# Optimization experiments

Measured on AMD Instinct MI355X. Metric: run time of the kernel, lower is better.

## Reference

```python
import jax, jax.numpy as jnp
from jax import lax
import numpy as np

B, T, L = 8, 24, 145
DHID, DFRAME, DEMB, DGCN, V = 1024, 2500, 128, 512, 1024
PF = 300
DINP = DHID + DFRAME + DEMB + DGCN   # 4164 = LSTM input size
DCONT = DHID + DINP                  # 5188 = cont_t size
FLAT = 64 * 7 * 7                    # 3136
BN_EPS = 1e-5
BN_INV = float(1.0 / np.sqrt(1.0 + BN_EPS))  # eval BN with running mean 0, var 1


def setup_inputs() -> dict:
    key = jax.random.key(0)
    ks = iter(jax.random.split(key, 48))
    rn = lambda *s: jax.random.normal(next(ks), s, jnp.float32)
    w = lambda *s: 0.02 * rn(*s)
    return dict(
        enc=rn(B, L, DHID),
        frames=rn(B, T, 512, 7, 7),
        gcn_embedding=rn(B, DGCN),
        h0=jnp.zeros((B, DHID), jnp.float32),
        c0=jnp.zeros((B, DHID), jnp.float32),
        conv1_w=w(256, 512), conv1_b=jnp.zeros((256,), jnp.float32),
        bn1_g=jnp.ones((256,), jnp.float32), bn1_b=jnp.zeros((256,), jnp.float32),
        conv2_w=w(64, 256), conv2_b=jnp.zeros((64,), jnp.float32),
        bn2_g=jnp.ones((64,), jnp.float32), bn2_b=jnp.zeros((64,), jnp.float32),
        fc_w=w(DFRAME, FLAT), fc_b=jnp.zeros((DFRAME,), jnp.float32),
        hfc_w=w(DHID, DHID), hfc_b=jnp.zeros((DHID,), jnp.float32),
        w_ih=w(4 * DHID, DINP), w_hh=w(4 * DHID, DHID),
        b_ih=jnp.zeros((4 * DHID,), jnp.float32), b_hh=jnp.zeros((4 * DHID,), jnp.float32),
        go=0.1 * rn(DEMB),
        emb_w=w(V, DEMB),
        actor_w=w(DEMB, DCONT), actor_b=jnp.zeros((DEMB,), jnp.float32),
        d1_w=w(FLAT, DCONT), d1_b=jnp.zeros((FLAT,), jnp.float32),
        dconv3_w=w(64, 32, 4, 4), dconv3_b=jnp.zeros((32,), jnp.float32),
        bnm2_g=jnp.ones((32,), jnp.float32), bnm2_b=jnp.zeros((32,), jnp.float32),
        dconv2_w=w(32, 16, 4, 4), dconv2_b=jnp.zeros((16,), jnp.float32),
        bnm1_g=jnp.ones((16,), jnp.float32), bnm1_b=jnp.zeros((16,), jnp.float32),
        dconv1_w=w(16, 1, 4, 4), dconv1_b=jnp.zeros((1,), jnp.float32),
    )


def _bn_eval(x, g, b):
    # BatchNorm2d in eval mode with running_mean=0, running_var=1
    return g[None, :, None, None] * (x * BN_INV) + b[None, :, None, None]


def _up2(x):
    # UpsamplingNearest2d(scale_factor=2)
    return jnp.repeat(jnp.repeat(x, 2, axis=2), 2, axis=3)


def _deconv(x, w, b):
    # ConvTranspose2d(k=4, s=2, p=1); torch weight layout (in, out, kH, kW)
    k = jnp.flip(w, (2, 3)).transpose(1, 0, 2, 3)  # -> (out, in, kH, kW)
    y = lax.conv_general_dilated(x, k, window_strides=(1, 1), padding=((2, 2), (2, 2)),
                                 lhs_dilation=(2, 2),
                                 dimension_numbers=('NCHW', 'OIHW', 'NCHW'))
    return y + b[None, :, None, None]


def reference(enc, frames, gcn_embedding, h0, c0,
              conv1_w, conv1_b, bn1_g, bn1_b, conv2_w, conv2_b, bn2_g, bn2_b, fc_w, fc_b,
              hfc_w, hfc_b, w_ih, w_hh, b_ih, b_hh, go, emb_w, actor_w, actor_b,
              d1_w, d1_b, dconv3_w, dconv3_b, bnm2_g, bnm2_b,
              dconv2_w, dconv2_b, bnm1_g, bnm1_b, dconv1_w, dconv1_b):

    def vis_encode(frame):  # [B,512,7,7] -> [B,DFRAME]
        x = jnp.einsum('bchw,oc->bohw', frame, conv1_w) + conv1_b[None, :, None, None]
        x = jax.nn.relu(_bn_eval(x, bn1_g, bn1_b))
        x = jnp.einsum('bchw,oc->bohw', x, conv2_w) + conv2_b[None, :, None, None]
        x = jax.nn.relu(_bn_eval(x, bn2_g, bn2_b))
        return x.reshape(-1, FLAT) @ fc_w.T + fc_b

    def mask_decode(cont):  # [B,DCONT] -> [B,1,300,300]
        x = jax.nn.relu(cont @ d1_w.T + d1_b).reshape(-1, 64, 7, 7)
        x = _deconv(_up2(x), dconv3_w, dconv3_b)          # 14 -> 28
        x = jax.nn.relu(_bn_eval(x, bnm2_g, bnm2_b))
        x = _deconv(_up2(x), dconv2_w, dconv2_b)          # 56 -> 112
        x = jax.nn.relu(_bn_eval(x, bnm1_g, bnm1_b))
        x = _deconv(x, dconv1_w, dconv1_b)                # 112 -> 224
        return jax.image.resize(x, (x.shape[0], 1, PF, PF), method='bilinear')

    def step(carry, frame_t):
        h, c, e_t = carry
        vis = vis_encode(frame_t)
        hq = h @ hfc_w.T + hfc_b
        score = jax.nn.softmax(jnp.einsum('bld,bd->bl', enc, hq), axis=1)  # [B,L]
        weighted = jnp.einsum('bl,bld->bd', score, enc)
        inp = jnp.concatenate([vis, weighted, e_t, gcn_embedding], axis=1)  # [B,DINP]
        gates = inp @ w_ih.T + b_ih + h @ w_hh.T + b_hh
        i, f, g, o = jnp.split(gates, 4, axis=1)
        c_new = jax.nn.sigmoid(f) * c + jax.nn.sigmoid(i) * jnp.tanh(g)
        h_new = jax.nn.sigmoid(o) * jnp.tanh(c_new)
        cont = jnp.concatenate([h_new, inp], axis=1)  # [B,DCONT]
        action = (cont @ actor_w.T + actor_b) @ emb_w.T  # [B,V]
        mask = mask_decode(cont)
        e_new = emb_w[jnp.argmax(action, axis=1)]  # greedy feed-back
        return (h_new, c_new, e_new), (action, mask, score[:, :, None])

    e0 = jnp.tile(go[None, :], (enc.shape[0], 1))
    (h_T, c_T, _), (actions, masks, attns) = lax.scan(
        step, (h0, c0, e0), jnp.swapaxes(frames, 0, 1))
    out_action = jnp.swapaxes(actions, 0, 1)   # [B,T,V]
    out_mask = jnp.swapaxes(masks, 0, 1)       # [B,T,1,300,300]
    out_attn = jnp.swapaxes(attns, 0, 1)       # [B,T,L,1]
    return (out_action, out_mask, out_attn, h_T, c_T)
```

## Files before the change

kernel.cpp:

```cpp
#include <hip/hip_runtime.h>
#include <cstdint>
#include <cstddef>

#define DEV __device__ __forceinline__
typedef short bf16x8 __attribute__((ext_vector_type(8)));
typedef float fl4 __attribute__((ext_vector_type(4)));
typedef float f32x4 __attribute__((ext_vector_type(4)));
typedef unsigned short u16;

#define BN_INV 0.9999950000375f

DEV float b2f(u16 u){ return __uint_as_float(((unsigned)u)<<16); }
DEV u16 f2b(float f){ unsigned u = __float_as_uint(f); unsigned r = (u + 0x7FFFu + ((u>>16)&1u))>>16; return (u16)r; }

DEV bf16x8 load8(const u16* p){ return *(const bf16x8*)p; }
DEV bf16x8 load8(const float* p){
  fl4 a = *(const fl4*)p; fl4 b = *(const fl4*)(p+4);
  bf16x8 r;
  r[0]=(short)f2b(a[0]); r[1]=(short)f2b(a[1]); r[2]=(short)f2b(a[2]); r[3]=(short)f2b(a[3]);
  r[4]=(short)f2b(b[0]); r[5]=(short)f2b(b[1]); r[6]=(short)f2b(b[2]); r[7]=(short)f2b(b[3]);
  return r;
}


__global__ __launch_bounds__(256) void k_pack_frames(const float* __restrict__ fr, u16* __restrict__ XT){
  int bt = blockIdx.x, tid = threadIdx.x;
  for (int e=0;e<128;e++){
    int flat = e*256 + tid;
    int p = flat>>9, c = flat&511;
    u16 v = 0;
    if (p < 49) v = f2b(fr[((size_t)bt*512 + c)*49 + p]);
    XT[((size_t)bt*64 + p)*512 + c] = v;
  }
}

__global__ __launch_bounds__(256) void k_pack_wseq(const float* __restrict__ w_ih, const float* __restrict__ w_hh,
                                                   u16* __restrict__ wseq){
  int r = blockIdx.x, tid = threadIdx.x;
  const float* wr = w_ih + (size_t)r*4164;
  for (int j=tid;j<2176;j+=256){
    float v = (j < 1024) ? w_hh[(size_t)r*1024 + j] : wr[2500 + (j-1024)];
    wseq[(size_t)r*2176 + j] = f2b(v);
  }
}

__global__ __launch_bounds__(256) void k_pack_dseq(const float* __restrict__ d1_w, const float* __restrict__ actor_w,
                                                   u16* __restrict__ dseq){
  int r = blockIdx.x, tid = threadIdx.x;
  const float* wr = (r < 3136) ? (d1_w + (size_t)r*5188) : (actor_w + (size_t)(r-3136)*5188);
  for (int j=tid;j<2176;j+=256){
    float v = (j < 1024) ? wr[j] : wr[3524 + (j-1024)];
    dseq[(size_t)r*2176 + j] = f2b(v);
  }
}

__global__ __launch_bounds__(256) void k_pack_fcw(const float* __restrict__ fc_w, u16* __restrict__ fcwB){
  int r = blockIdx.x, tid = threadIdx.x;
  const float* wr = fc_w + (size_t)r*3136;
  u16* dst = fcwB + (size_t)r*3136;
  for (int j=tid;j<3136;j+=256) dst[j] = f2b(wr[j]);
}

__global__ __launch_bounds__(256) void k_pack_wvg(const float* __restrict__ w_ih, u16* __restrict__ wvg, int rbase){
  int r = rbase + blockIdx.x, tid = threadIdx.x;
  const float* wr = w_ih + (size_t)r*4164;
  u16* dst = wvg + (size_t)blockIdx.x*3072;
  for (int j=tid;j<3072;j+=256){
    float v = 0.f;
    if (j < 2500) v = wr[j];
    else if (j < 3012) v = wr[3652 + (j-2500)];
    dst[j] = f2b(v);
  }
}

__global__ __launch_bounds__(256) void k_pack_dvg(const float* __restrict__ d1_w, const float* __restrict__ actor_w,
                                                  u16* __restrict__ dvg, int rbase){
  int r = rbase + blockIdx.x, tid = threadIdx.x;
  const float* wr = (r < 3136) ? (d1_w + (size_t)r*5188) : (actor_w + (size_t)(r-3136)*5188);
  u16* dst = dvg + (size_t)blockIdx.x*3072;
  for (int j=tid;j<3072;j+=256){
    float v = 0.f;
    if (j < 2500) v = wr[1024 + j];
    else if (j < 3012) v = wr[4676 + (j-2500)];
    dst[j] = f2b(v);
  }
}

__global__ __launch_bounds__(256) void k_hfcT(const float* __restrict__ hfc_w, u16* __restrict__ hfcT){
  int idx = blockIdx.x*256 + threadIdx.x;
  int k = idx>>10, o = idx&1023;
  hfcT[idx] = f2b(hfc_w[o*1024 + k]);
}

DEV u16 wt_map(const float* w, int n, int k, int CIN, int COUT){
  int o = n % COUT; int cls = n / COUT;
  if (cls >= 4) return 0;
  int py = cls>>1, px = cls&1;
  int i = k/9; int dd = k - i*9; int dy = dd/3, dx = dd - dy*3;
  if (i >= CIN) return 0;
  int ky = (py==0) ? (dy==0 ? 3 : (dy==1 ? 1 : -1)) : (dy==1 ? 2 : (dy==2 ? 0 : -1));
  int kx = (px==0) ? (dx==0 ? 3 : (dx==1 ? 1 : -1)) : (dx==1 ? 2 : (dx==2 ? 0 : -1));
  if (ky < 0 || kx < 0) return 0;
  return f2b(w[((i*COUT + o)*4 + ky)*4 + kx]);
}

__global__ __launch_bounds__(256) void k_misc(
  const float* b_ih, const float* b_hh, const float* d1_b, const float* actor_b,
  const float* emb_w, const float* h0, const float* c0,
  const float* dw3, const float* dw2, const float* dw1,
  float* bias_g, float* bias_da, u16* embT, float* hb0, float* cws,
  u16* Wt3, u16* Wt2, u16* Wt1)
{
  int blk = blockIdx.x, tid = threadIdx.x;
  if (blk < 16){ int i = blk*256+tid; if (i<4096) bias_g[i] = b_ih[i] + b_hh[i]; }
  else if (blk < 29){ int i = (blk-16)*256+tid; if (i<3264) bias_da[i] = (i<3136)? d1_b[i] : actor_b[i-3136]; }
  else if (blk < 541){ int i = (blk-29)*256+tid; int j = i>>10, v = i&1023; embT[i] = f2b(emb_w[v*128 + j]); }
  else if (blk < 573){ int i = (blk-541)*256+tid; if (i<8192){ hb0[i] = h0[i]; cws[i] = c0[i]; } }
  else if (blk < 574){ for (int i=tid;i<2560;i+=256){ int n=i/160, k=i-n*160; Wt1[i] = wt_map(dw1,n,k,16,1); } }
  else if (blk < 590){ for (int i=(blk-574)*256+tid; i<18432; i+=16*256){ int n=i/288, k=i-n*288; Wt2[i] = wt_map(dw2,n,k,32,16); } }
  else { for (int i=(blk-590)*256+tid; i<73728; i+=168*256){ int n=i/576, k=i-n*576; Wt3[i] = wt_map(dw3,n,k,64,32); } }
}

__global__ __launch_bounds__(256) void k_eb(const float* __restrict__ enc, const float* __restrict__ hfc_b, float* __restrict__ eb){
  int li = blockIdx.x*4 + (threadIdx.x>>6);
  int lane = threadIdx.x & 63;
  if (li >= 1160) return;
  const float* ep = enc + (size_t)li*1024;
  float a = 0.f;
  for (int k=lane;k<1024;k+=64) a += ep[k]*hfc_b[k];
  #pragma unroll
  for (int off=32; off; off>>=1) a += __shfl_xor(a, off);
  if (lane == 0) eb[li] = a;
}

__global__ __launch_bounds__(256) void k_vis_in(const u16* __restrict__ Y2, u16* __restrict__ vis_in){
  int bt = blockIdx.x, tid = threadIdx.x;
  for (int f=tid; f<3136; f+=256){
    int c = f/49, p = f - c*49;
    vis_in[(size_t)bt*3136 + f] = Y2[((size_t)bt*64 + p)*64 + c];
  }
}

__global__ __launch_bounds__(256) void k_xin(const u16* __restrict__ vis, const float* __restrict__ gcn, u16* __restrict__ xin2){
  int bt = blockIdx.x, tid = threadIdx.x, b = bt/24;
  for (int j=tid;j<3072;j+=256){
    u16 v = 0;
    if (j < 2500) v = vis[(size_t)bt*2500 + j];
    else if (j < 3012) v = f2b(gcn[b*512 + (j-2500)]);
    xin2[(size_t)bt*3072 + j] = v;
  }
}

template<int OUTB, int ACT, typename TA, typename TB>
__global__ __launch_bounds__(256) void gemm64(
  const TA* __restrict__ A, int lda, const TB* __restrict__ Bm, int ldb,
  void* __restrict__ Cv, int ldc, int M, int N, int K,
  const float* __restrict__ bias, const float* __restrict__ cb, const float* __restrict__ gg, const float* __restrict__ bb)
{
  __shared__ u16 sA[64*72];
  __shared__ u16 sB[64*72];
  int tid = threadIdx.x, lane = tid & 63, w = tid >> 6;
  int wm = w & 1, wn = w >> 1;
  int m0 = blockIdx.x*64, n0 = blockIdx.y*64;
  f32x4 acc[2][2];
  #pragma unroll
  for (int a=0;a<2;a++)
    #pragma unroll
    for (int b=0;b<2;b++){ acc[a][b][0]=0;acc[a][b][1]=0;acc[a][b][2]=0;acc[a][b][3]=0; }

  for (int k0=0;k0<K;k0+=64){
    #pragma unroll
    for (int j=0;j<2;j++){
      int c = tid + 256*j; int row = c>>3; int col = (c&7)*8;
      bf16x8 va = {0,0,0,0,0,0,0,0};
      int gm = m0 + row;
      if (gm < M) va = load8(A + (size_t)gm*lda + k0 + col);
      *(bf16x8*)(&sA[row*72 + col]) = va;
      bf16x8 vb = {0,0,0,0,0,0,0,0};
      int gn = n0 + row;
      if (gn < N) vb = load8(Bm + (size_t)gn*ldb + k0 + col);
      *(bf16x8*)(&sB[row*72 + col]) = vb;
    }
    __syncthreads();
    #pragma unroll
    for (int kk=0;kk<2;kk++){
      bf16x8 af[2], bfv[2];
      #pragma unroll
      for (int tm=0;tm<2;tm++) af[tm]  = *(const bf16x8*)(&sA[(wm*32+tm*16+(lane&15))*72 + kk*32 + (lane>>4)*8]);
      #pragma unroll
      for (int tn=0;tn<2;tn++) bfv[tn] = *(const bf16x8*)(&sB[(wn*32+tn*16+(lane&15))*72 + kk*32 + (lane>>4)*8]);
      #pragma unroll
      for (int tm=0;tm<2;tm++)
        #pragma unroll
        for (int tn=0;tn<2;tn++)
          acc[tm][tn] = __builtin_amdgcn_mfma_f32_16x16x32_bf16(af[tm], bfv[tn], acc[tm][tn], 0,0,0);
    }
    __syncthreads();
  }
  int ml = (lane>>4)*4, nl = lane&15;
  #pragma unroll
  for (int tm=0;tm<2;tm++)
    #pragma unroll
    for (int tn=0;tn<2;tn++)
      #pragma unroll
      for (int r=0;r<4;r++){
        int gm = m0 + wm*32 + tm*16 + ml + r;
        int gn = n0 + wn*32 + tn*16 + nl;
        if (gm < M && gn < N){
          float v = acc[tm][tn][r];
          if (ACT == 0){ if (bias) v += bias[gn]; }
          else { v = (v + cb[gn])*BN_INV*gg[gn] + bb[gn]; v = fmaxf(v, 0.f); }
          if (OUTB) ((u16*)Cv)[(size_t)gm*ldc + gn] = f2b(v);
          else      ((float*)Cv)[(size_t)gm*ldc + gn] = v;
        }
      }
}

template<int OUTB, int NMAJOR, typename TA, typename TB>
__global__ __launch_bounds__(64) void gemm16x(
  const TA* __restrict__ A, int lda, const TB* __restrict__ Bm, int ldb,
  void* __restrict__ Cv, int ldc, int M, int N, int K, const float* __restrict__ bias,
  int MT, int NT)
{
  int nb = gridDim.x;
  int orig = blockIdx.x;
  int q = nb >> 3, r = nb & 7;
  int xcd = orig & 7, j = orig >> 3;
  int wg = (xcd < r ? xcd*(q+1) : r*(q+1) + (xcd-r)*q) + j;
  int bx, by;
  if (NMAJOR){ bx = wg % MT; by = wg / MT; }
  else       { by = wg % NT; bx = wg / NT; }
  int lane = threadIdx.x;
  int m0 = bx*16, n0 = by*16;
  int gm = m0 + (lane&15); if (gm > M-1) gm = M-1;
  int gn = n0 + (lane&15); if (gn > N-1) gn = N-1;
  const TA* ap = A  + (size_t)gm*lda + ((lane>>4)*8);
  const TB* bp = Bm + (size_t)gn*ldb + ((lane>>4)*8);
  f32x4 acc = {0,0,0,0};
  #pragma unroll 8
  for (int ks=0; ks<K; ks+=32){
    bf16x8 a = load8(ap + ks);
    bf16x8 b = load8(bp + ks);
    acc = __builtin_amdgcn_mfma_f32_16x16x32_bf16(a, b, acc, 0,0,0);
  }
  int nn = n0 + (lane&15);
  if (nn >= N) return;
  #pragma unroll
  for (int r2=0;r2<4;r2++){
    int mm = m0 + (lane>>4)*4 + r2;
    if (mm < M){
      float v = acc[r2];
      if (bias) v += bias[nn];
      if (OUTB) ((u16*)Cv)[(size_t)mm*ldc + nn] = f2b(v);
      else      ((float*)Cv)[(size_t)mm*ldc + nn] = v;
    }
  }
}


__global__ __launch_bounds__(256) void p1_scores_action(
  const float* __restrict__ encH, const float* __restrict__ eb,
  const float* __restrict__ hcur, const float* __restrict__ cws,
  float* __restrict__ scores, const float* __restrict__ d1a_out,
  const u16* __restrict__ embT, float* __restrict__ out_act,
  float* __restrict__ cmv, int* __restrict__ cmi,
  float* __restrict__ out_h, float* __restrict__ out_c,
  u16* __restrict__ xb1, int t)
{
  __shared__ float shf[1024];
  __shared__ int shi[256];
  int blk = blockIdx.x, tid = threadIdx.x;
  if (blk < 40){
    if (t == 24) return;
    int b = blk & 7, lc = blk >> 3;
    #pragma unroll
    for (int e=0;e<4;e++) shf[tid + 256*e] = hcur[b*1024 + tid + 256*e];
    __syncthreads();
    int w = tid>>6, lane = tid&63;
    for (int i=w;i<29;i+=4){
      int l = lc*29 + i;
      const float* ep = encH + (size_t)(b*145+l)*1024;
      float a = 0.f;
      for (int k=lane;k<1024;k+=64) a += ep[k]*shf[k];
      #pragma unroll
      for (int off=32; off; off>>=1) a += __shfl_xor(a, off);
      if (lane == 0) scores[b*145+l] = a + eb[b*145+l];
    }
  } else if (blk < 72){
    if (t == 0) return;
    int idx = blk-40; int b = idx>>2, vc = idx&3;
    if (tid < 128) shf[tid] = d1a_out[(size_t)(b*24 + t-1)*3264 + 3136 + tid];
    __syncthreads();
    int v = vc*256 + tid;
    float a = 0.f;
    for (int j=0;j<128;j++) a += shf[j]*b2f(embT[j*1024 + v]);
    out_act[(size_t)(b*24 + t-1)*1024 + v] = a;
    shf[256+tid] = a; shi[tid] = v;
    __syncthreads();
    for (int s=128; s; s>>=1){
      if (tid < s){
        float o = shf[256+tid+s]; int oi = shi[tid+s];
        float c = shf[256+tid];   int ci = shi[tid];
        if (o > c || (o == c && oi < ci)){ shf[256+tid] = o; shi[tid] = oi; }
      }
      __syncthreads();
    }
    if (tid == 0){ cmv[b*4+vc] = shf[256]; cmi[b*4+vc] = shi[0]; }
  } else {
    int b = blk-72;
    if (t == 24){
      #pragma unroll
      for (int e=0;e<4;e++){
        int k = tid + 256*e;
        out_h[b*1024+k] = hcur[b*1024+k];
        out_c[b*1024+k] = cws[b*1024+k];
      }
    } else {
      #pragma unroll
      for (int e=0;e<4;e++){
        int k = tid + 256*e;
        xb1[b*2176 + k] = f2b(hcur[b*1024+k]);
      }
    }
  }
}

__global__ __launch_bounds__(256) void p2_softmax_weighted(
  const float* __restrict__ scores, const float* __restrict__ enc,
  float* __restrict__ wgt, float* __restrict__ ecur,
  const float* __restrict__ cmv, const int* __restrict__ cmi,
  const float* __restrict__ emb_w, const float* __restrict__ go,
  float* __restrict__ out_attn, u16* __restrict__ xb1, u16* __restrict__ xb2, int t)
{
  int b = blockIdx.x & 7, dc = blockIdx.x >> 3, tid = threadIdx.x;
  __shared__ float s[145];
  __shared__ float mxs, invs;
  if (tid < 145) s[tid] = scores[b*145+tid];
  __syncthreads();
  if (tid < 64){
    float m = -1e30f;
    for (int i=tid;i<145;i+=64) m = fmaxf(m, s[i]);
    #pragma unroll
    for (int off=32; off; off>>=1) m = fmaxf(m, __shfl_xor(m, off));
    if (tid == 0) mxs = m;
  }
  __syncthreads();
  if (tid < 145) s[tid] = expf(s[tid]-mxs);
  __syncthreads();
  if (tid < 64){
    float sm = 0.f;
    for (int i=tid;i<145;i+=64) sm += s[i];
    #pragma unroll
    for (int off=32; off; off>>=1) sm += __shfl_xor(sm, off);
    if (tid == 0) invs = 1.f/sm;
  }
  __syncthreads();
  float inv = invs;
  if (tid < 128){
    int d = dc*128 + tid;
    float a = 0.f;
    for (int l=0;l<145;l++) a += s[l]*enc[(size_t)(b*145+l)*1024 + d];
    float wv = a*inv;
    wgt[b*1024+d] = wv;
    u16 wb = f2b(wv);
    xb1[b*2176 + 1024 + d] = wb;
    xb2[b*2176 + 1024 + d] = wb;
  } else {
    int i = tid-128;
    if (dc == 0){
      if (i < 145) out_attn[(size_t)(b*24+t)*145 + i] = s[i]*inv;
      int l2 = i + 128;
      if (l2 < 145) out_attn[(size_t)(b*24+t)*145 + l2] = s[l2]*inv;
    } else if (dc == 1){
      float ev;
      if (t == 0) ev = go[i];
      else {
        float bv = cmv[b*4]; int bi = cmi[b*4];
        #pragma unroll
        for (int c=1;c<4;c++){
          float v2 = cmv[b*4+c]; int i2 = cmi[b*4+c];
          if (v2 > bv || (v2 == bv && i2 < bi)){ bv = v2; bi = i2; }
        }
        ev = emb_w[bi*128 + i];
      }
      ecur[b*128+i] = ev;
      u16 eb16 = f2b(ev);
      xb1[b*2176 + 2048 + i] = eb16;
      xb2[b*2176 + 2048 + i] = eb16;
    }
  }
}

__global__ __launch_bounds__(64) void p3m(
  const u16* __restrict__ wseq, const u16* __restrict__ xb, float* __restrict__ gates4)
{
  int orig = blockIdx.x;
  int blk = (orig & 7)*32 + (orig >> 3);
  int lane = threadIdx.x;
  int n = blk*16 + (lane & 15);
  const u16* bp = wseq + (size_t)n*2176 + ((lane>>4)*8);
  const u16* ap = xb + (lane&7)*2176 + ((lane>>4)*8);
  f32x4 acc = {0,0,0,0};
  #pragma unroll 8
  for (int kk=0;kk<68;kk++){
    bf16x8 a = *(const bf16x8*)(ap + kk*32);
    bf16x8 b = *(const bf16x8*)(bp + kk*32);
    acc = __builtin_amdgcn_mfma_f32_16x16x32_bf16(a, b, acc, 0,0,0);
  }
  #pragma unroll
  for (int r=0;r<4;r++){
    int m = (lane>>4)*4 + r;
    if (m < 8) gates4[(size_t)m*4096 + n] = acc[r];
  }
}

__global__ __launch_bounds__(256) void p3l(
  const float* __restrict__ gates4, const float* __restrict__ gpre,
  float* __restrict__ hnew, float* __restrict__ cws, u16* __restrict__ xb2, int t)
{
  int idx = blockIdx.x*256 + threadIdx.x;
  int b = idx>>10, J = idx&1023;
  const float* gp = gpre + (size_t)(b*24+t)*4096;
  const float* gb = gates4 + (size_t)b*4096;
  float iv = gb[J]      + gp[J];
  float fv = gb[1024+J] + gp[1024+J];
  float gv = gb[2048+J] + gp[2048+J];
  float ov = gb[3072+J] + gp[3072+J];
  float ig = 1.f/(1.f+expf(-iv));
  float fg = 1.f/(1.f+expf(-fv));
  float gt = tanhf(gv);
  float og = 1.f/(1.f+expf(-ov));
  float cn = fg*cws[idx] + ig*gt;
  cws[idx] = cn;
  float hv = og*tanhf(cn);
  hnew[idx] = hv;
  xb2[b*2176 + J] = f2b(hv);
}

__global__ __launch_bounds__(64) void p4m(
  const u16* __restrict__ dseq, const u16* __restrict__ xb2,
  const float* __restrict__ dpre, float* __restrict__ dout, int t)
{
  int orig = blockIdx.x;
  int xcd = orig & 7, j = orig >> 3;
  int blk = (xcd < 4 ? xcd*26 : 104 + (xcd-4)*25) + j;
  int lane = threadIdx.x;
  int R = blk*16 + (lane & 15);
  const u16* bp = dseq + (size_t)R*2176 + ((lane>>4)*8);
  const u16* ap = xb2 + (lane&7)*2176 + ((lane>>4)*8);
  f32x4 acc = {0,0,0,0};
  #pragma unroll 8
  for (int kk=0;kk<68;kk++){
    bf16x8 a = *(const bf16x8*)(ap + kk*32);
    bf16x8 b = *(const bf16x8*)(bp + kk*32);
    acc = __builtin_amdgcn_mfma_f32_16x16x32_bf16(a, b, acc, 0,0,0);
  }
  #pragma unroll
  for (int r=0;r<4;r++){
    int m = (lane>>4)*4 + r;
    if (m < 8){
      size_t row = (size_t)(m*24+t)*3264;
      dout[row + R] = acc[r] + dpre[row + R];
    }
  }
}


DEV void stage_tile3(u16* sAt, const float* __restrict__ d1a_bt, int p0, int tid){
  int m = tid & 15;
  int p = p0 + m;
  int u = p / 14, v = p - u*14;
  bool pv = p < 196;
  for (int k = tid>>4; k < 576; k += 16){
    float val = 0.f;
    if (pv){
      int i = k/9; int dd = k - i*9; int dy = dd/3, dx = dd - dy*3;
      int uy = u + dy - 1, vx = v + dx - 1;
      if (uy >= 0 && uy < 14 && vx >= 0 && vx < 14)
        val = fmaxf(d1a_bt[i*49 + (uy>>1)*7 + (vx>>1)], 0.f);
    }
    sAt[m*584 + k] = f2b(val);
  }
}

DEV void stage_tile2(u16* sAt, const float* __restrict__ m1c_bt, int p0, int tid){
  int m = tid & 15;
  int p = p0 + m;
  int u = p / 56, v = p - u*56;
  bool pv = p < 3136;
  for (int k = tid>>4; k < 288; k += 16){
    float val = 0.f;
    if (pv){
      int i = k/9; int dd = k - i*9; int dy = dd/3, dx = dd - dy*3;
      int uy = u + dy - 1, vx = v + dx - 1;
      if (uy >= 0 && uy < 56 && vx >= 0 && vx < 56)
        val = m1c_bt[i*784 + (uy>>1)*28 + (vx>>1)];
    }
    sAt[m*296 + k] = f2b(val);
  }
}

__global__ __launch_bounds__(256) void md3_deconv(const float* __restrict__ d1a_out, int btbase, float* __restrict__ m1c,
  const u16* __restrict__ Wt3, const float* __restrict__ b3, const float* __restrict__ g3, const float* __restrict__ bb3)
{
  __shared__ u16 sAt[16*584];
  int tid = threadIdx.x, lane = tid&63, w = tid>>6;
  int cb = blockIdx.x;
  const float* in_bt = d1a_out + (size_t)(btbase+cb)*3264;
  float* out_bt = m1c + (size_t)cb*32*784;
  int nt = blockIdx.y*4 + w;
  bf16x8 wc[18];
  #pragma unroll
  for (int ks=0;ks<18;ks++) wc[ks] = *(const bf16x8*)(Wt3 + (size_t)(nt*16 + (lane&15))*576 + ks*32 + (lane>>4)*8);
  int cls = nt>>1; int o = (nt&1)*16 + (lane&15);
  int py = cls>>1, px = cls&1;
  float cbv = b3[o], gv = g3[o], bbv = bb3[o];
  int mt = blockIdx.z;
  stage_tile3(sAt, in_bt, mt*16, tid);
  __syncthreads();
  f32x4 acc = {0,0,0,0};
  #pragma unroll
  for (int ks=0;ks<18;ks++){
    bf16x8 a = *(const bf16x8*)(&sAt[(lane&15)*584 + ks*32 + (lane>>4)*8]);
    acc = __builtin_amdgcn_mfma_f32_16x16x32_bf16(a, wc[ks], acc, 0,0,0);
  }
  #pragma unroll
  for (int r=0;r<4;r++){
    int p = mt*16 + (lane>>4)*4 + r;
    if (p < 196){
      int u = p/14, v = p - (p/14)*14;
      float vv = fmaxf((acc[r] + cbv)*BN_INV*gv + bbv, 0.f);
      out_bt[((size_t)o*28 + (2*u+py))*28 + (2*v+px)] = vv;
    }
  }
}

__global__ __launch_bounds__(256) void md2_deconv(const float* __restrict__ m1c, float* __restrict__ m2,
  const u16* __restrict__ Wt2, const float* __restrict__ b2, const float* __restrict__ g2, const float* __restrict__ bb2)
{
  __shared__ u16 sAt[16*296];
  int tid = threadIdx.x, lane = tid&63, w = tid>>6;
  int cb = blockIdx.x;
  const float* in_bt = m1c + (size_t)cb*32*784;
  float* out_bt = m2 + (size_t)cb*16*12544;
  int nt = w;
  bf16x8 wc[9];
  #pragma unroll
  for (int ks=0;ks<9;ks++) wc[ks] = *(const bf16x8*)(Wt2 + (size_t)(nt*16 + (lane&15))*288 + ks*32 + (lane>>4)*8);
  int cls = nt; int o = lane&15;
  int py = cls>>1, px = cls&1;
  float cbv = b2[o], gv = g2[o], bbv = bb2[o];
  int mt = blockIdx.y;
  stage_tile2(sAt, in_bt, mt*16, tid);
  __syncthreads();
  f32x4 acc = {0,0,0,0};
  #pragma unroll
  for (int ks=0;ks<9;ks++){
    bf16x8 a = *(const bf16x8*)(&sAt[(lane&15)*296 + ks*32 + (lane>>4)*8]);
    acc = __builtin_amdgcn_mfma_f32_16x16x32_bf16(a, wc[ks], acc, 0,0,0);
  }
  #pragma unroll
  for (int r=0;r<4;r++){
    int p = mt*16 + (lane>>4)*4 + r;
    if (p < 3136){
      int u = p/56, v = p - u*56;
      float vv = fmaxf((acc[r] + cbv)*BN_INV*gv + bbv, 0.f);
      out_bt[((size_t)o*112 + (2*u+py))*112 + (2*v+px)] = vv;
    }
  }
}

__global__ __launch_bounds__(256) void md1_direct(const float* __restrict__ m2, float* __restrict__ m3,
  const float* __restrict__ dw1, const float* __restrict__ b1)
{
  __shared__ float wl[256];
  int tid = threadIdx.x;
  wl[tid] = dw1[tid];
  __syncthreads();
  int cb = blockIdx.x;
  const float* in_bt = m2 + (size_t)cb*16*12544;
  float* out_bt = m3 + (size_t)cb*50176;
  int idx = blockIdx.y*256 + tid;
  int oy = idx/56, q = idx - oy*56;
  int ox0 = q*4;
  int iyA = (oy+1)>>1;  bool vA = iyA < 112;
  int iyB = iyA - 1;    bool vB = iyB >= 0;
  int kyA = (oy&1) ? 0 : 1;
  int kyB = kyA + 2;
  int xb = (ox0>>1) - 1;
  bool v0 = xb >= 0, v3 = (xb+3) < 112;
  int x0 = v0 ? xb : 0, x3 = v3 ? xb+3 : 111;
  float mA = vA ? 1.f : 0.f, mB = vB ? 1.f : 0.f;
  float mA0 = v0 ? mA : 0.f, mA3 = v3 ? mA : 0.f;
  float mB0 = v0 ? mB : 0.f, mB3 = v3 ? mB : 0.f;
  const float* rA = in_bt + (size_t)(vA ? iyA : 0)*112;
  const float* rB = in_bt + (size_t)(vB ? iyB : 0)*112;
  float acc0=0.f, acc1=0.f, acc2=0.f, acc3=0.f;
  #pragma unroll 4
  for (int i=0;i<16;i++){
    const float* cA = rA + i*12544;
    const float* cB = rB + i*12544;
    float a0 = cA[x0]*mA0, a1 = cA[xb+1]*mA, a2 = cA[xb+2]*mA, a3 = cA[x3]*mA3;
    float b0 = cB[x0]*mB0, b1v = cB[xb+1]*mB, b2 = cB[xb+2]*mB, b3 = cB[x3]*mB3;
    fl4 wA = *(const fl4*)(&wl[i*16 + kyA*4]);
    fl4 wB = *(const fl4*)(&wl[i*16 + kyB*4]);
    acc0 += a1*wA[1] + a0*wA[3] + b1v*wB[1] + b0*wB[3];
    acc1 += a2*wA[0] + a1*wA[2] + b2*wB[0] + b1v*wB[2];
    acc2 += a2*wA[1] + a1*wA[3] + b2*wB[1] + b1v*wB[3];
    acc3 += a3*wA[0] + a2*wA[2] + b3*wB[0] + b2*wB[2];
  }
  float bv = b1[0];
  fl4 o4 = {acc0+bv, acc1+bv, acc2+bv, acc3+bv};
  *(fl4*)(out_bt + (size_t)oy*224 + ox0) = o4;
}

__global__ __launch_bounds__(256) void k_resize(const float* __restrict__ m3, float* __restrict__ out_mask, int btbase){
  int cb = blockIdx.x;
  const float* in_bt = m3 + (size_t)cb*50176;
  int idx = blockIdx.y*256 + threadIdx.x;
  if (idx >= 90000) return;
  int oy = idx/300, ox = idx - oy*300;
  const float sc = 224.f/300.f;
  float sy = (oy+0.5f)*sc - 0.5f;
  float sx = (ox+0.5f)*sc - 0.5f;
  float fy = floorf(sy), fx = floorf(sx);
  float wy = sy-fy, wx = sx-fx;
  int y0 = (int)fy, x0 = (int)fx;
  int y0c = min(max(y0,0),223), y1c = min(max(y0+1,0),223);
  int x0c = min(max(x0,0),223), x1c = min(max(x0+1,0),223);
  float v00 = in_bt[y0c*224+x0c], v01 = in_bt[y0c*224+x1c];
  float v10 = in_bt[y1c*224+x0c], v11 = in_bt[y1c*224+x1c];
  float v = (1.f-wy)*((1.f-wx)*v00 + wx*v01) + wy*((1.f-wx)*v10 + wx*v11);
  out_mask[(size_t)(btbase+cb)*90000 + idx] = v;
}


extern "C" void kernel_launch(void* const* d_in, const int* in_sizes, int n_in,
                              void* d_out, int out_size, void* d_ws, size_t ws_size,
                              hipStream_t stream)
{
  const float* enc      = (const float*)d_in[0];
  const float* frames   = (const float*)d_in[1];
  const float* gcn      = (const float*)d_in[2];
  const float* h0       = (const float*)d_in[3];
  const float* c0       = (const float*)d_in[4];
  const float* conv1_w  = (const float*)d_in[5];
  const float* conv1_b  = (const float*)d_in[6];
  const float* bn1_g    = (const float*)d_in[7];
  const float* bn1_b    = (const float*)d_in[8];
  const float* conv2_w  = (const float*)d_in[9];
  const float* conv2_b  = (const float*)d_in[10];
  const float* bn2_g    = (const float*)d_in[11];
  const float* bn2_b    = (const float*)d_in[12];
  const float* fc_w     = (const float*)d_in[13];
  const float* fc_b     = (const float*)d_in[14];
  const float* hfc_w    = (const float*)d_in[15];
  const float* hfc_b    = (const float*)d_in[16];
  const float* w_ih     = (const float*)d_in[17];
  const float* w_hh     = (const float*)d_in[18];
  const float* b_ih     = (const float*)d_in[19];
  const float* b_hh     = (const float*)d_in[20];
  const float* go       = (const float*)d_in[21];
  const float* emb_w    = (const float*)d_in[22];
  const float* actor_w  = (const float*)d_in[23];
  const float* actor_b  = (const float*)d_in[24];
  const float* d1_w     = (const float*)d_in[25];
  const float* d1_b     = (const float*)d_in[26];
  const float* dconv3_w = (const float*)d_in[27];
  const float* dconv3_b = (const float*)d_in[28];
  const float* bnm2_g   = (const float*)d_in[29];
  const float* bnm2_b   = (const float*)d_in[30];
  const float* dconv2_w = (const float*)d_in[31];
  const float* dconv2_b = (const float*)d_in[32];
  const float* bnm1_g   = (const float*)d_in[33];
  const float* bnm1_b   = (const float*)d_in[34];
  const float* dconv1_w = (const float*)d_in[35];
  const float* dconv1_b = (const float*)d_in[36];
  (void)in_sizes; (void)n_in; (void)out_size;

  float* obase    = (float*)d_out;
  float* out_act  = obase;
  float* out_mask = obase + 196608;
  float* out_attn = obase + 17476608;
  float* out_h    = obase + 17504448;
  float* out_c    = obase + 17512640;

  char* ob = (char*)out_mask;
  size_t ooff = 0;
  auto oalloc = [&](size_t bytes)->char*{ char* p = ob + ooff; ooff = (ooff + bytes + 255) & ~(size_t)255; return p; };
  u16*   wseq      = (u16*)  oalloc(4096ULL*2176*2);
  u16*   dseq      = (u16*)  oalloc(3264ULL*2176*2);
  float* encH      = (float*)oalloc(1160ULL*1024*4);
  float* gates_pre = (float*)oalloc(192ULL*4096*4);
  float* d1a_pre   = (float*)oalloc(192ULL*3264*4);
  u16*   xin2      = (u16*)  oalloc(192ULL*3072*2);
  u16*   XT     = (u16*)oalloc(12288ULL*512*2);
  u16*   Y1     = (u16*)oalloc(12288ULL*256*2);
  u16*   Y2     = (u16*)oalloc(12288ULL*64*2);
  u16*   vis_in = (u16*)oalloc(192ULL*3136*2);
  u16*   vis    = (u16*)oalloc(192ULL*2500*2);
  u16*   wchunk = XT;
  u16*   fcwB   = XT;

  char* wsb = (char*)d_ws;
  size_t off = 0;
  auto alloc = [&](size_t bytes)->char*{ char* p = wsb + off; off = (off + bytes + 255) & ~(size_t)255; return p; };
  float* d1a_out   = (float*)alloc(192ULL*3264*4);
  u16*   embT      = (u16*)  alloc(128ULL*1024*2);
  float* eb        = (float*)alloc(1160ULL*4);
  u16*   Wt3       = (u16*)  alloc(128ULL*576*2);
  u16*   Wt2       = (u16*)  alloc(64ULL*288*2);
  u16*   Wt1       = (u16*)  alloc(16ULL*160*2);
  float* hb        = (float*)alloc(2ULL*8192*4);
  float* c_ws      = (float*)alloc(8192ULL*4);
  float* e_cur     = (float*)alloc(8ULL*128*4);
  float* weighted  = (float*)alloc(8192ULL*4);
  float* scores_raw= (float*)alloc(8ULL*145*4);
  float* cmv       = (float*)alloc(32ULL*4);
  int*   cmi       = (int*)  alloc(32ULL*4);
  float* bias_g    = (float*)alloc(4096ULL*4);
  float* bias_da   = (float*)alloc(3264ULL*4);
  u16*   xb1       = (u16*)  alloc(8ULL*2176*2);
  u16*   xb2       = (u16*)  alloc(8ULL*2176*2);
  float* gates4    = (float*)alloc(8ULL*4096*4);
  size_t zbase = off;
  u16*   hfcT = (u16*)alloc(1024ULL*1024*2);

  const int cands[10] = {48,24,16,12,8,6,4,3,2,1};
  int C = 1;
  for (int i=0;i<10;i++){
    size_t need = zbase + (size_t)cands[i]*1103872ULL + 65536;
    if (need <= ws_size){ C = cands[i]; break; }
  }
  size_t mo = zbase;
  auto malloc_ = [&](size_t bytes)->char*{ char* p = wsb + mo; mo = (mo + bytes + 255) & ~(size_t)255; return p; };
  float* m1c  = (float*)malloc_((size_t)C*32*784*4);
  float* m2b  = (float*)malloc_((size_t)C*16*12544*4);
  float* m3b  = (float*)malloc_((size_t)C*50176*4);

  k_pack_frames<<<192, 256, 0, stream>>>(frames, XT);
  k_pack_wseq<<<4096, 256, 0, stream>>>(w_ih, w_hh, wseq);
  k_pack_dseq<<<3264, 256, 0, stream>>>(d1_w, actor_w, dseq);
  k_hfcT<<<4096, 256, 0, stream>>>(hfc_w, hfcT);
  k_misc<<<758, 256, 0, stream>>>(b_ih, b_hh, d1_b, actor_b, emb_w, h0, c0,
                                  dconv3_w, dconv2_w, dconv1_w,
                                  bias_g, bias_da, embT, hb, c_ws, Wt3, Wt2, Wt1);
  k_eb<<<290, 256, 0, stream>>>(enc, hfc_b, eb);

  gemm64<1,1><<<dim3(192,4), 256, 0, stream>>>(XT, 512, conv1_w, 512, Y1, 256, 12288, 256, 512, nullptr, conv1_b, bn1_g, bn1_b);
  gemm64<1,1><<<dim3(192,1), 256, 0, stream>>>(Y1, 256, conv2_w, 256, Y2, 64, 12288, 64, 256, nullptr, conv2_b, bn2_g, bn2_b);
  k_vis_in<<<192, 256, 0, stream>>>(Y2, vis_in);
  k_pack_fcw<<<2500, 256, 0, stream>>>(fc_w, fcwB);
  gemm16x<1,1><<<12*157, 64, 0, stream>>>(vis_in, 3136, fcwB, 3136, vis, 2500, 192, 2500, 3136, fc_b, 12, 157);
  k_xin<<<192, 256, 0, stream>>>(vis, gcn, xin2);
  gemm16x<0,0><<<73*64, 64, 0, stream>>>(enc, 1024, hfcT, 1024, encH, 1024, 1160, 1024, 1024, nullptr, 73, 64);

  for (int c=0;c<2;c++){
    k_pack_wvg<<<2048, 256, 0, stream>>>(w_ih, wchunk, c*2048);
    gemm16x<0,1><<<12*128, 64, 0, stream>>>(xin2, 3072, wchunk, 3072, gates_pre + c*2048, 4096,
                                            192, 2048, 3072, bias_g + c*2048, 12, 128);
  }
  for (int c=0;c<2;c++){
    k_pack_dvg<<<1632, 256, 0, stream>>>(d1_w, actor_w, wchunk, c*1632);
    gemm16x<0,1><<<12*102, 64, 0, stream>>>(xin2, 3072, wchunk, 3072, d1a_pre + c*1632, 3264,
                                            192, 1632, 3072, bias_da + c*1632, 12, 102);
  }

  for (int t=0; t<=24; t++){
    float* hcur = hb + (t&1)*8192;
    float* hnew = hb + ((t+1)&1)*8192;
    p1_scores_action<<<80, 256, 0, stream>>>(encH, eb, hcur, c_ws, scores_raw, d1a_out, embT,
                                             out_act, cmv, cmi, out_h, out_c, xb1, t);
    if (t == 24) break;
    p2_softmax_weighted<<<64, 256, 0, stream>>>(scores_raw, enc, weighted, e_cur, cmv, cmi, emb_w, go,
                                                out_attn, xb1, xb2, t);
    p3m<<<256, 64, 0, stream>>>(wseq, xb1, gates4);
    p3l<<<32, 256, 0, stream>>>(gates4, gates_pre, hnew, c_ws, xb2, t);
    p4m<<<204, 64, 0, stream>>>(dseq, xb2, d1a_pre, d1a_out, t);
  }

  for (int btbase=0; btbase<192; btbase+=C){
    md3_deconv<<<dim3(C,2,13), 256, 0, stream>>>(d1a_out, btbase, m1c, Wt3, dconv3_b, bnm2_g, bnm2_b);
    md2_deconv<<<dim3(C,196), 256, 0, stream>>>(m1c, m2b, Wt2, dconv2_b, bnm1_g, bnm1_b);
    md1_direct<<<dim3(C,49), 256, 0, stream>>>(m2b, m3b, dconv1_w, dconv1_b);
    k_resize<<<dim3(C,352), 256, 0, stream>>>(m3b, out_mask, btbase);
  }
}
```

Measured before the change: 2.925 ms.

## Fuse LSTM gate GEMM with cell update and stage mask decoder in bf16

Merges the recurrent gate matvec and the LSTM pointwise kernel into one block-per-hidden-slice kernel. Each block computes all four gates for its 16 hidden units and applies the cell update from shared memory, which removes a launch and the gates4 round trip on every timestep. The d1 output is also written as ReLU'd bf16 so the deconv stages read half-size inputs. Staging now gathers the 3x3 upsampled neighbourhood from four loads instead of per-k index math, md3 covers all 8 n-tiles in one 512-thread block, and m1 is stored in bf16. In exchange the gate kernel has only 64 blocks of 4 waves, and storing intermediates in bf16 adds a small rounding change.

After: 3.038 ms. +3.8%, slower.

```diff
diff --git a/kernel.cpp b/kernel.cpp
--- a/kernel.cpp
+++ b/kernel.cpp
@@ -391,15 +391,17 @@
   }
 }
 
-__global__ __launch_bounds__(64) void p3m(
-  const u16* __restrict__ wseq, const u16* __restrict__ xb, float* __restrict__ gates4)
-{
+__global__ __launch_bounds__(256) void p3f(
+  const u16* __restrict__ wseq, const u16* __restrict__ xb1, const float* __restrict__ gpre,
+  float* __restrict__ hnew, float* __restrict__ cws, u16* __restrict__ xb2, int t)
+{
+  __shared__ float gl[512];
+  int tid = threadIdx.x, lane = tid & 63, g = tid >> 6;
   int orig = blockIdx.x;
-  int blk = (orig & 7)*32 + (orig >> 3);
-  int lane = threadIdx.x;
-  int n = blk*16 + (lane & 15);
+  int nb = (orig & 7)*8 + (orig >> 3);
+  int n = g*1024 + nb*16 + (lane & 15);
   const u16* bp = wseq + (size_t)n*2176 + ((lane>>4)*8);
-  const u16* ap = xb + (lane&7)*2176 + ((lane>>4)*8);
+  const u16* ap = xb1 + (lane&7)*2176 + ((lane>>4)*8);
   f32x4 acc = {0,0,0,0};
   #pragma unroll 8
   for (int kk=0;kk<68;kk++){
@@ -410,36 +412,31 @@
   #pragma unroll
   for (int r=0;r<4;r++){
     int m = (lane>>4)*4 + r;
-    if (m < 8) gates4[(size_t)m*4096 + n] = acc[r];
-  }
-}
-
-__global__ __launch_bounds__(256) void p3l(
-  const float* __restrict__ gates4, const float* __restrict__ gpre,
-  float* __restrict__ hnew, float* __restrict__ cws, u16* __restrict__ xb2, int t)
-{
-  int idx = blockIdx.x*256 + threadIdx.x;
-  int b = idx>>10, J = idx&1023;
-  const float* gp = gpre + (size_t)(b*24+t)*4096;
-  const float* gb = gates4 + (size_t)b*4096;
-  float iv = gb[J]      + gp[J];
-  float fv = gb[1024+J] + gp[1024+J];
-  float gv = gb[2048+J] + gp[2048+J];
-  float ov = gb[3072+J] + gp[3072+J];
-  float ig = 1.f/(1.f+expf(-iv));
-  float fg = 1.f/(1.f+expf(-fv));
-  float gt = tanhf(gv);
-  float og = 1.f/(1.f+expf(-ov));
-  float cn = fg*cws[idx] + ig*gt;
-  cws[idx] = cn;
-  float hv = og*tanhf(cn);
-  hnew[idx] = hv;
-  xb2[b*2176 + J] = f2b(hv);
+    if (m < 8) gl[(g*16 + (lane&15))*8 + m] = acc[r];
+  }
+  __syncthreads();
+  if (tid < 128){
+    int j = tid>>3, b = tid&7; int J = nb*16 + j;
+    const float* gp = gpre + (size_t)(b*24+t)*4096;
+    float iv = gl[(0*16+j)*8+b] + gp[J];
+    float fv = gl[(1*16+j)*8+b] + gp[1024+J];
+    float gv = gl[(2*16+j)*8+b] + gp[2048+J];
+    float ov = gl[(3*16+j)*8+b] + gp[3072+J];
+    float ig = 1.f/(1.f+expf(-iv));
+    float fg = 1.f/(1.f+expf(-fv));
+    float gt = tanhf(gv);
+    float og = 1.f/(1.f+expf(-ov));
+    float cn = fg*cws[b*1024+J] + ig*gt;
+    cws[b*1024+J] = cn;
+    float hv = og*tanhf(cn);
+    hnew[b*1024+J] = hv;
+    xb2[b*2176 + J] = f2b(hv);
+  }
 }
 
 __global__ __launch_bounds__(64) void p4m(
   const u16* __restrict__ dseq, const u16* __restrict__ xb2,
-  const float* __restrict__ dpre, float* __restrict__ dout, int t)
+  const float* __restrict__ dpre, float* __restrict__ dout, u16* __restrict__ d1b, int t)
 {
   int orig = blockIdx.x;
   int xcd = orig & 7, j = orig >> 3;
@@ -460,63 +457,81 @@
     int m = (lane>>4)*4 + r;
     if (m < 8){
       size_t row = (size_t)(m*24+t)*3264;
-      dout[row + R] = acc[r] + dpre[row + R];
-    }
-  }
-}
-
-
-DEV void stage_tile3(u16* sAt, const float* __restrict__ d1a_bt, int p0, int tid){
-  int m = tid & 15;
+      float v = acc[r] + dpre[row + R];
+      dout[row + R] = v;
+      if (R < 3136) d1b[(size_t)(m*24+t)*3136 + R] = f2b(fmaxf(v, 0.f));
+    }
+  }
+}
+
+
+DEV void stage3b(u16* sAt, const u16* __restrict__ d1b_bt, int p0, int tid){
+  int m = tid & 15, j = tid >> 4;
   int p = p0 + m;
   int u = p / 14, v = p - u*14;
   bool pv = p < 196;
-  for (int k = tid>>4; k < 576; k += 16){
-    float val = 0.f;
-    if (pv){
-      int i = k/9; int dd = k - i*9; int dy = dd/3, dx = dd - dy*3;
-      int uy = u + dy - 1, vx = v + dx - 1;
-      if (uy >= 0 && uy < 14 && vx >= 0 && vx < 14)
-        val = fmaxf(d1a_bt[i*49 + (uy>>1)*7 + (vx>>1)], 0.f);
-    }
-    sAt[m*584 + k] = f2b(val);
-  }
-}
-
-DEV void stage_tile2(u16* sAt, const float* __restrict__ m1c_bt, int p0, int tid){
-  int m = tid & 15;
+  int rA=(u-1)>>1, rB=(u+1)>>1, cA=(v-1)>>1, cB=(v+1)>>1;
+  int rAc = rA<0?0:rA, rBc = rB>6?6:rB, cAc = cA<0?0:cA, cBc = cB>6?6:cB;
+  bool y0 = pv && (u>=1), y2 = pv && (u<13), y1 = pv;
+  bool x0 = (v>=1), x2 = (v<13);
+  bool uodd = (u&1), vodd = (v&1);
+  #pragma unroll
+  for (int i2=0;i2<2;i2++){
+    int i = j*2 + i2;
+    const u16* b = d1b_bt + i*49;
+    u16 aa=b[rAc*7+cAc], ab=b[rAc*7+cBc], ba=b[rBc*7+cAc], bb=b[rBc*7+cBc];
+    u16 r0a = y0?aa:(u16)0, r0b = y0?ab:(u16)0;
+    u16 r2a = y2?ba:(u16)0, r2b = y2?bb:(u16)0;
+    u16 r1a = uodd?aa:ba,   r1b = uodd?ab:bb;
+    r1a = y1?r1a:(u16)0;    r1b = y1?r1b:(u16)0;
+    u16* dst = sAt + m*584 + i*9;
+    dst[0]= x0?r0a:(u16)0; dst[1]= vodd?r0a:r0b; dst[2]= x2?r0b:(u16)0;
+    dst[3]= x0?r1a:(u16)0; dst[4]= vodd?r1a:r1b; dst[5]= x2?r1b:(u16)0;
+    dst[6]= x0?r2a:(u16)0; dst[7]= vodd?r2a:r2b; dst[8]= x2?r2b:(u16)0;
+  }
+}
+
+DEV void stage2b(u16* sAt, const u16* __restrict__ m1b_bt, int p0, int tid){
+  int m = tid & 15, j = tid >> 4;
   int p = p0 + m;
   int u = p / 56, v = p - u*56;
-  bool pv = p < 3136;
-  for (int k = tid>>4; k < 288; k += 16){
-    float val = 0.f;
-    if (pv){
-      int i = k/9; int dd = k - i*9; int dy = dd/3, dx = dd - dy*3;
-      int uy = u + dy - 1, vx = v + dx - 1;
-      if (uy >= 0 && uy < 56 && vx >= 0 && vx < 56)
-        val = m1c_bt[i*784 + (uy>>1)*28 + (vx>>1)];
-    }
-    sAt[m*296 + k] = f2b(val);
-  }
-}
-
-__global__ __launch_bounds__(256) void md3_deconv(const float* __restrict__ d1a_out, int btbase, float* __restrict__ m1c,
+  int rA=(u-1)>>1, rB=(u+1)>>1, cA=(v-1)>>1, cB=(v+1)>>1;
+  int rAc = rA<0?0:rA, rBc = rB>27?27:rB, cAc = cA<0?0:cA, cBc = cB>27?27:cB;
+  bool y0 = (u>=1), y2 = (u<55);
+  bool x0 = (v>=1), x2 = (v<55);
+  bool uodd = (u&1), vodd = (v&1);
+  #pragma unroll
+  for (int i2=0;i2<2;i2++){
+    int i = j*2 + i2;
+    const u16* b = m1b_bt + i*784;
+    u16 aa=b[rAc*28+cAc], ab=b[rAc*28+cBc], ba=b[rBc*28+cAc], bb=b[rBc*28+cBc];
+    u16 r0a = y0?aa:(u16)0, r0b = y0?ab:(u16)0;
+    u16 r2a = y2?ba:(u16)0, r2b = y2?bb:(u16)0;
+    u16 r1a = uodd?aa:ba,   r1b = uodd?ab:bb;
+    u16* dst = sAt + m*296 + i*9;
+    dst[0]= x0?r0a:(u16)0; dst[1]= vodd?r0a:r0b; dst[2]= x2?r0b:(u16)0;
+    dst[3]= x0?r1a:(u16)0; dst[4]= vodd?r1a:r1b; dst[5]= x2?r1b:(u16)0;
+    dst[6]= x0?r2a:(u16)0; dst[7]= vodd?r2a:r2b; dst[8]= x2?r2b:(u16)0;
+  }
+}
+
+__global__ __launch_bounds__(512) void md3_deconv(const u16* __restrict__ d1b, int btbase, u16* __restrict__ m1b,
   const u16* __restrict__ Wt3, const float* __restrict__ b3, const float* __restrict__ g3, const float* __restrict__ bb3)
 {
   __shared__ u16 sAt[16*584];
   int tid = threadIdx.x, lane = tid&63, w = tid>>6;
   int cb = blockIdx.x;
-  const float* in_bt = d1a_out + (size_t)(btbase+cb)*3264;
-  float* out_bt = m1c + (size_t)cb*32*784;
-  int nt = blockIdx.y*4 + w;
+  const u16* in_bt = d1b + (size_t)(btbase+cb)*3136;
+  u16* out_bt = m1b + (size_t)cb*32*784;
+  int nt = w;
   bf16x8 wc[18];
   #pragma unroll
   for (int ks=0;ks<18;ks++) wc[ks] = *(const bf16x8*)(Wt3 + (size_t)(nt*16 + (lane&15))*576 + ks*32 + (lane>>4)*8);
   int cls = nt>>1; int o = (nt&1)*16 + (lane&15);
   int py = cls>>1, px = cls&1;
   float cbv = b3[o], gv = g3[o], bbv = bb3[o];
-  int mt = blockIdx.z;
-  stage_tile3(sAt, in_bt, mt*16, tid);
+  int mt = blockIdx.y;
+  stage3b(sAt, in_bt, mt*16, tid);
   __syncthreads();
   f32x4 acc = {0,0,0,0};
   #pragma unroll
@@ -530,18 +545,18 @@
     if (p < 196){
       int u = p/14, v = p - (p/14)*14;
       float vv = fmaxf((acc[r] + cbv)*BN_INV*gv + bbv, 0.f);
-      out_bt[((size_t)o*28 + (2*u+py))*28 + (2*v+px)] = vv;
-    }
-  }
-}
-
-__global__ __launch_bounds__(256) void md2_deconv(const float* __restrict__ m1c, float* __restrict__ m2,
+      out_bt[((size_t)o*28 + (2*u+py))*28 + (2*v+px)] = f2b(vv);
+    }
+  }
+}
+
+__global__ __launch_bounds__(256) void md2_deconv(const u16* __restrict__ m1b, float* __restrict__ m2,
   const u16* __restrict__ Wt2, const float* __restrict__ b2, const float* __restrict__ g2, const float* __restrict__ bb2)
 {
   __shared__ u16 sAt[16*296];
   int tid = threadIdx.x, lane = tid&63, w = tid>>6;
   int cb = blockIdx.x;
-  const float* in_bt = m1c + (size_t)cb*32*784;
+  const u16* in_bt = m1b + (size_t)cb*32*784;
   float* out_bt = m2 + (size_t)cb*16*12544;
   int nt = w;
   bf16x8 wc[9];
@@ -551,7 +566,7 @@
   int py = cls>>1, px = cls&1;
   float cbv = b2[o], gv = g2[o], bbv = bb2[o];
   int mt = blockIdx.y;
-  stage_tile2(sAt, in_bt, mt*16, tid);
+  stage2b(sAt, in_bt, mt*16, tid);
   __syncthreads();
   f32x4 acc = {0,0,0,0};
   #pragma unroll
@@ -706,6 +721,7 @@
   size_t off = 0;
   auto alloc = [&](size_t bytes)->char*{ char* p = wsb + off; off = (off + bytes + 255) & ~(size_t)255; return p; };
   float* d1a_out   = (float*)alloc(192ULL*3264*4);
+  u16*   d1b       = (u16*)  alloc(192ULL*3136*2);
   u16*   embT      = (u16*)  alloc(128ULL*1024*2);
   float* eb        = (float*)alloc(1160ULL*4);
   u16*   Wt3       = (u16*)  alloc(128ULL*576*2);
@@ -722,19 +738,18 @@
   float* bias_da   = (float*)alloc(3264ULL*4);
   u16*   xb1       = (u16*)  alloc(8ULL*2176*2);
   u16*   xb2       = (u16*)  alloc(8ULL*2176*2);
-  float* gates4    = (float*)alloc(8ULL*4096*4);
   size_t zbase = off;
   u16*   hfcT = (u16*)alloc(1024ULL*1024*2);
 
   const int cands[10] = {48,24,16,12,8,6,4,3,2,1};
   int C = 1;
   for (int i=0;i<10;i++){
-    size_t need = zbase + (size_t)cands[i]*1103872ULL + 65536;
+    size_t need = zbase + (size_t)cands[i]*1053696ULL + 65536;
     if (need <= ws_size){ C = cands[i]; break; }
   }
   size_t mo = zbase;
   auto malloc_ = [&](size_t bytes)->char*{ char* p = wsb + mo; mo = (mo + bytes + 255) & ~(size_t)255; return p; };
-  float* m1c  = (float*)malloc_((size_t)C*32*784*4);
+  u16*   m1b  = (u16*)  malloc_((size_t)C*32*784*2);
   float* m2b  = (float*)malloc_((size_t)C*16*12544*4);
   float* m3b  = (float*)malloc_((size_t)C*50176*4);
 
@@ -774,14 +789,13 @@
     if (t == 24) break;
     p2_softmax_weighted<<<64, 256, 0, stream>>>(scores_raw, enc, weighted, e_cur, cmv, cmi, emb_w, go,
                                                 out_attn, xb1, xb2, t);
-    p3m<<<256, 64, 0, stream>>>(wseq, xb1, gates4);
-    p3l<<<32, 256, 0, stream>>>(gates4, gates_pre, hnew, c_ws, xb2, t);
-    p4m<<<204, 64, 0, stream>>>(dseq, xb2, d1a_pre, d1a_out, t);
+    p3f<<<64, 256, 0, stream>>>(wseq, xb1, gates_pre, hnew, c_ws, xb2, t);
+    p4m<<<204, 64, 0, stream>>>(dseq, xb2, d1a_pre, d1a_out, d1b, t);
   }
 
   for (int btbase=0; btbase<192; btbase+=C){
-    md3_deconv<<<dim3(C,2,13), 256, 0, stream>>>(d1a_out, btbase, m1c, Wt3, dconv3_b, bnm2_g, bnm2_b);
-    md2_deconv<<<dim3(C,196), 256, 0, stream>>>(m1c, m2b, Wt2, dconv2_b, bnm1_g, bnm1_b);
+    md3_deconv<<<dim3(C,13), 512, 0, stream>>>(d1b, btbase, m1b, Wt3, dconv3_b, bnm2_g, bnm2_b);
+    md2_deconv<<<dim3(C,196), 256, 0, stream>>>(m1b, m2b, Wt2, dconv2_b, bnm1_g, bnm1_b);
     md1_direct<<<dim3(C,49), 256, 0, stream>>>(m2b, m3b, dconv1_w, dconv1_b);
     k_resize<<<dim3(C,352), 256, 0, stream>>>(m3b, out_mask, btbase);
   }
```
